# Kernel optimization log

Measured on AMD Instinct MI355X. Metric: run time of the kernel, lower is better.

## Reference

```python
import jax, jax.numpy as jnp
import numpy as np

GROUP = 128  # per-group quantization along the input dimension


def _quantize_int4(w):
    """Asymmetric INT4 per-group quantization. w: [out, in] -> (q, scale, zero).
    q: int32 in [0,15], shape [out, in//GROUP, GROUP]; scale/zero: [out, in//GROUP]."""
    o, i = w.shape
    wg = w.reshape(o, i // GROUP, GROUP)
    mn = wg.min(axis=-1)
    mx = wg.max(axis=-1)
    scale = (mx - mn) / 15.0
    scale = jnp.where(scale == 0, jnp.float32(1.0), scale)
    zero = jnp.clip(jnp.round(-mn / scale), 0.0, 15.0)
    q = jnp.clip(jnp.round(wg / scale[..., None]) + zero[..., None], 0.0, 15.0).astype(jnp.int32)
    return q, scale.astype(jnp.float32), zero.astype(jnp.float32)


def _dequant(q, s, z):
    """(q - zero) * scale, regrouped back to [out, in]."""
    w = (q.astype(jnp.float32) - z[..., None]) * s[..., None]
    return w.reshape(q.shape[0], -1)


def setup_inputs() -> dict:
    key = jax.random.key(0)
    ks = jax.random.split(key, 5)
    B, D_IN, D_H, D_OUT = 512, 2048, 8192, 2048
    x = jax.random.normal(ks[0], (B, D_IN), dtype=jnp.float32)
    w1 = jax.random.normal(ks[1], (D_H, D_IN), dtype=jnp.float32) * 0.02
    b1 = jax.random.normal(ks[2], (D_H,), dtype=jnp.float32) * 0.01
    w2 = jax.random.normal(ks[3], (D_OUT, D_H), dtype=jnp.float32) * 0.02
    b2 = jax.random.normal(ks[4], (D_OUT,), dtype=jnp.float32) * 0.01
    q1, s1, z1 = _quantize_int4(w1)
    q2, s2, z2 = _quantize_int4(w2)
    return {"x": x, "q1": q1, "s1": s1, "z1": z1, "b1": b1,
            "q2": q2, "s2": s2, "z2": z2, "b2": b2}


def reference(x, q1, s1, z1, b1, q2, s2, z2, b2):
    # Layer 1: INT4 dequant + Linear + ReLU (fused in the native kernel)
    w1 = _dequant(q1, s1, z1)              # [D_H, D_IN]
    h = jax.nn.relu(x @ w1.T + b1)         # [B, D_H]
    # Layer 2: INT4 dequant + Linear (no activation)
    w2 = _dequant(q2, s2, z2)              # [D_OUT, D_H]
    return h @ w2.T + b2                   # [B, D_OUT]
```

## Files before the change

### kernel.cpp

```cpp
#include <hip/hip_runtime.h>
#include <stdint.h>

typedef unsigned short u16;
typedef __attribute__((ext_vector_type(8))) short bf16x8;
typedef __attribute__((ext_vector_type(8))) unsigned short u16x8;
typedef __attribute__((ext_vector_type(4))) float f32x4;
typedef __attribute__((ext_vector_type(4))) int i32x4;

__device__ __forceinline__ u16 f2bf(float f) {
  uint32_t u = __builtin_bit_cast(uint32_t, f);
  u += 0x7fffu + ((u >> 16) & 1u);
  return (u16)(u >> 16);
}

#define GLD16(g, l)                                                         \
  __builtin_amdgcn_global_load_lds(                                         \
      (const __attribute__((address_space(1))) void*)(g),                   \
      (__attribute__((address_space(3))) void*)(l), 16, 0, 0)


__global__ __launch_bounds__(256) void cvt_f32_bf16(const float* __restrict__ src,
                                                    u16* __restrict__ dst, int n8) {
  int t = blockIdx.x * 256 + threadIdx.x;
  if (t >= n8) return;
  f32x4 a = ((const f32x4*)src)[2 * t];
  f32x4 b = ((const f32x4*)src)[2 * t + 1];
  u16x8 o;
  o[0] = f2bf(a[0]); o[1] = f2bf(a[1]); o[2] = f2bf(a[2]); o[3] = f2bf(a[3]);
  o[4] = f2bf(b[0]); o[5] = f2bf(b[1]); o[6] = f2bf(b[2]); o[7] = f2bf(b[3]);
  ((u16x8*)dst)[t] = o;
}

__global__ __launch_bounds__(256) void dequant_w(const int* __restrict__ q,
                                                 const float* __restrict__ s,
                                                 const float* __restrict__ z,
                                                 u16* __restrict__ w, int n8) {
  int t = blockIdx.x * 256 + threadIdx.x;
  if (t >= n8) return;
  int g = t >> 4;
  float sc = s[g];
  float zp = z[g];
  i32x4 a = ((const i32x4*)q)[2 * t];
  i32x4 b = ((const i32x4*)q)[2 * t + 1];
  u16x8 o;
  o[0] = f2bf(((float)a[0] - zp) * sc);
  o[1] = f2bf(((float)a[1] - zp) * sc);
  o[2] = f2bf(((float)a[2] - zp) * sc);
  o[3] = f2bf(((float)a[3] - zp) * sc);
  o[4] = f2bf(((float)b[0] - zp) * sc);
  o[5] = f2bf(((float)b[1] - zp) * sc);
  o[6] = f2bf(((float)b[2] - zp) * sc);
  o[7] = f2bf(((float)b[3] - zp) * sc);
  ((u16x8*)w)[t] = o;
}

__global__ __launch_bounds__(256) void bias_init(float* __restrict__ out,
                                                 const float* __restrict__ b,
                                                 int N, int n4) {
  int t = blockIdx.x * 256 + threadIdx.x;
  if (t >= n4) return;
  int idx = t * 4;
  int n = idx & (N - 1);
  *(f32x4*)(out + idx) = *(const f32x4*)(b + n);
}

template <bool RELU, bool OUT_BF16, bool ATOMIC>
__global__ __launch_bounds__(256) void gemm_bt(const u16* __restrict__ A,
                                               const u16* __restrict__ Bm,
                                               const float* __restrict__ bias,
                                               void* __restrict__ Cout,
                                               int M, int N, int K, int kChunk) {
  __shared__ u16 As[3][128 * 32];
  __shared__ u16 Bs[3][128 * 32];
  const int tid = threadIdx.x;
  const int wave = tid >> 6;
  const int lane = tid & 63;
  const int m0 = blockIdx.y << 7;
  const int n0 = blockIdx.x << 7;
  const int kStart = blockIdx.z * kChunk;
  const int srow = lane >> 2;
  const int scol = (((lane & 3) ^ ((lane >> 3) & 3)) << 3);
  const int wm = (wave >> 1) << 6;
  const int wn = (wave & 1) << 6;
  const int quad = lane >> 4;
  const int l15 = lane & 15;
  const int cs = ((quad ^ ((l15 >> 1) & 3)) << 3);

  const u16* Ab = A + (size_t)(m0 + 32 * wave + srow) * K + kStart + scol;
  const u16* Bb = Bm + (size_t)(n0 + 32 * wave + srow) * K + kStart + scol;
  const int ldsW = (32 * wave) * 32;
  const size_t rowskip = (size_t)16 * K;
  const int nT = kChunk >> 5;

  f32x4 acc[4][4];
#pragma unroll
  for (int i = 0; i < 4; i++)
#pragma unroll
    for (int j = 0; j < 4; j++) acc[i][j] = (f32x4){0.f, 0.f, 0.f, 0.f};

#define STAGE(bi_, t_)                                    \
  do {                                                    \
    const int ko_ = (t_) << 5;                            \
    GLD16(Ab + ko_, &As[bi_][ldsW]);                      \
    GLD16(Ab + ko_ + rowskip, &As[bi_][ldsW + 512]);      \
    GLD16(Bb + ko_, &Bs[bi_][ldsW]);                      \
    GLD16(Bb + ko_ + rowskip, &Bs[bi_][ldsW + 512]);      \
  } while (0)

  bf16x8 af[4], bf[4];
#define LOADFRAGS(bi_)                                                        \
  do {                                                                        \
    _Pragma("unroll") for (int i = 0; i < 4; i++)                             \
        af[i] = *(const bf16x8*)&As[bi_][(wm + i * 16 + l15) * 32 + cs];      \
    _Pragma("unroll") for (int j = 0; j < 4; j++)                             \
        bf[j] = *(const bf16x8*)&Bs[bi_][(wn + j * 16 + l15) * 32 + cs];      \
  } while (0)

#define DOMFMA()                                                              \
  do {                                                                        \
    _Pragma("unroll") for (int i = 0; i < 4; i++)                             \
        _Pragma("unroll") for (int j = 0; j < 4; j++)                         \
            acc[i][j] = __builtin_amdgcn_mfma_f32_16x16x32_bf16(              \
                af[i], bf[j], acc[i][j], 0, 0, 0);                            \
  } while (0)

  STAGE(0, 0);
  STAGE(1, 1);
  STAGE(2, 2);

  int bi = 0;
  for (int t = 0; t < nT - 2; ++t) {
    asm volatile("s_waitcnt vmcnt(8)" ::: "memory");
    __builtin_amdgcn_s_barrier();
    LOADFRAGS(bi);
    asm volatile("s_waitcnt lgkmcnt(0)" ::: "memory");
    __builtin_amdgcn_s_barrier();
    if (t + 3 < nT) STAGE(bi, t + 3);
    DOMFMA();
    bi = (bi == 2) ? 0 : bi + 1;
  }
  asm volatile("s_waitcnt vmcnt(4)" ::: "memory");
  __builtin_amdgcn_s_barrier();
  LOADFRAGS(bi);
  DOMFMA();
  bi = (bi == 2) ? 0 : bi + 1;
  asm volatile("s_waitcnt vmcnt(0)" ::: "memory");
  __builtin_amdgcn_s_barrier();
  LOADFRAGS(bi);
  DOMFMA();

#undef STAGE
#undef LOADFRAGS
#undef DOMFMA

#pragma unroll
  for (int i = 0; i < 4; i++) {
#pragma unroll
    for (int j = 0; j < 4; j++) {
      const int col = n0 + wn + j * 16 + l15;
      float bv = 0.f;
      if (!ATOMIC) bv = bias[col];
#pragma unroll
      for (int r = 0; r < 4; r++) {
        const int row = m0 + wm + i * 16 + quad * 4 + r;
        float v = acc[i][j][r];
        if (ATOMIC) {
          atomicAdd((float*)Cout + (size_t)row * N + col, v);
        } else {
          v += bv;
          if (RELU) v = v > 0.f ? v : 0.f;
          if (OUT_BF16)
            ((u16*)Cout)[(size_t)row * N + col] = f2bf(v);
          else
            ((float*)Cout)[(size_t)row * N + col] = v;
        }
      }
    }
  }
}


extern "C" void kernel_launch(void* const* d_in, const int* in_sizes, int n_in,
                              void* d_out, int out_size, void* d_ws, size_t ws_size,
                              hipStream_t stream) {
  const float* x  = (const float*)d_in[0];
  const int*   q1 = (const int*)d_in[1];
  const float* s1 = (const float*)d_in[2];
  const float* z1 = (const float*)d_in[3];
  const float* b1 = (const float*)d_in[4];
  const int*   q2 = (const int*)d_in[5];
  const float* s2 = (const float*)d_in[6];
  const float* z2 = (const float*)d_in[7];
  const float* b2 = (const float*)d_in[8];
  float* out = (float*)d_out;

  const int B = 512, D_IN = 2048, D_H = 8192, D_OUT = 2048;

  char* ws = (char*)d_ws;
  u16* xb  = (u16*)(ws);
  u16* w1b = (u16*)(ws + (size_t)2 * 1024 * 1024);
  u16* hb  = (u16*)(ws + (size_t)34 * 1024 * 1024);
  u16* w2b = (u16*)(ws + (size_t)42 * 1024 * 1024);

  cvt_f32_bf16<<<(B * D_IN / 8 + 255) / 256, 256, 0, stream>>>(x, xb, B * D_IN / 8);
  dequant_w<<<(D_H * D_IN / 8 + 255) / 256, 256, 0, stream>>>(q1, s1, z1, w1b, D_H * D_IN / 8);
  dequant_w<<<(D_OUT * D_H / 8 + 255) / 256, 256, 0, stream>>>(q2, s2, z2, w2b, D_OUT * D_H / 8);
  dim3 g1(D_H / 128, B / 128, 1);
  gemm_bt<true, true, false><<<g1, 256, 0, stream>>>(xb, w1b, b1, hb, B, D_H, D_IN, D_IN);
  bias_init<<<(B * D_OUT / 4 + 255) / 256, 256, 0, stream>>>(out, b2, D_OUT, B * D_OUT / 4);
  dim3 g2(D_OUT / 128, B / 128, 8);
  gemm_bt<false, false, true><<<g2, 256, 0, stream>>>(hb, w2b, nullptr, out, B, D_OUT, D_H, D_H / 8);
}
```

Baseline: 252.9 us.

## Merge dequant launches, narrow GEMM1 N-tile, double-buffer LDS, raise split-K

The two weight dequant launches become one launch with a z-dimension selecting the weight set. The GEMM becomes templated on N-tile width: GEMM1 uses 128x64 tiles to double the block count, and GEMM2's split-K rises from 8 to 16. The LDS pipeline drops from triple to double buffering, with sched_barriers added around the waits. These changes aim for more parallelism and occupancy, but they bring more atomic traffic in GEMM2 and less prefetch depth.

```diff
diff --git a/kernel.cpp b/kernel.cpp
--- a/kernel.cpp
+++ b/kernel.cpp
@@ -31,12 +31,20 @@
   ((u16x8*)dst)[t] = o;
 }
 
-__global__ __launch_bounds__(256) void dequant_w(const int* __restrict__ q,
-                                                 const float* __restrict__ s,
-                                                 const float* __restrict__ z,
-                                                 u16* __restrict__ w, int n8) {
+__global__ __launch_bounds__(256) void dequant_w2x(const int* __restrict__ qa,
+                                                   const float* __restrict__ sa,
+                                                   const float* __restrict__ za,
+                                                   u16* __restrict__ wa,
+                                                   const int* __restrict__ qb,
+                                                   const float* __restrict__ sb,
+                                                   const float* __restrict__ zb,
+                                                   u16* __restrict__ wb, int n8) {
   int t = blockIdx.x * 256 + threadIdx.x;
   if (t >= n8) return;
+  const int* q = blockIdx.z ? qb : qa;
+  const float* s = blockIdx.z ? sb : sa;
+  const float* z = blockIdx.z ? zb : za;
+  u16* w = blockIdx.z ? wb : wa;
   int g = t >> 4;
   float sc = s[g];
   float zp = z[g];
@@ -64,89 +72,92 @@
   *(f32x4*)(out + idx) = *(const f32x4*)(b + n);
 }
 
-template <bool RELU, bool OUT_BF16, bool ATOMIC>
+template <int NJ, bool RELU, bool OUT_BF16, bool ATOMIC>
 __global__ __launch_bounds__(256) void gemm_bt(const u16* __restrict__ A,
                                                const u16* __restrict__ Bm,
                                                const float* __restrict__ bias,
                                                void* __restrict__ Cout,
-                                               int M, int N, int K, int kChunk) {
-  __shared__ u16 As[3][128 * 32];
-  __shared__ u16 Bs[3][128 * 32];
+                                               int N, int K, int kChunk) {
+  __shared__ u16 As[2][128 * 32];
+  __shared__ u16 Bs[2][32 * NJ * 32];
   const int tid = threadIdx.x;
   const int wave = tid >> 6;
   const int lane = tid & 63;
   const int m0 = blockIdx.y << 7;
-  const int n0 = blockIdx.x << 7;
+  const int n0 = blockIdx.x * (32 * NJ);
   const int kStart = blockIdx.z * kChunk;
   const int srow = lane >> 2;
   const int scol = (((lane & 3) ^ ((lane >> 3) & 3)) << 3);
   const int wm = (wave >> 1) << 6;
-  const int wn = (wave & 1) << 6;
+  const int wn = (wave & 1) * (16 * NJ);
   const int quad = lane >> 4;
   const int l15 = lane & 15;
   const int cs = ((quad ^ ((l15 >> 1) & 3)) << 3);
 
   const u16* Ab = A + (size_t)(m0 + 32 * wave + srow) * K + kStart + scol;
-  const u16* Bb = Bm + (size_t)(n0 + 32 * wave + srow) * K + kStart + scol;
-  const int ldsW = (32 * wave) * 32;
+  const u16* Bb = Bm + (size_t)(n0 + (8 * NJ) * wave + srow) * K + kStart + scol;
+  const int ldsA = (32 * wave) * 32;
+  const int ldsB = ((8 * NJ) * wave) * 32;
   const size_t rowskip = (size_t)16 * K;
   const int nT = kChunk >> 5;
-
-  f32x4 acc[4][4];
+  constexpr int VM = 2 + NJ / 2;
+
+  f32x4 acc[4][NJ];
 #pragma unroll
   for (int i = 0; i < 4; i++)
 #pragma unroll
-    for (int j = 0; j < 4; j++) acc[i][j] = (f32x4){0.f, 0.f, 0.f, 0.f};
-
-#define STAGE(bi_, t_)                                    \
-  do {                                                    \
-    const int ko_ = (t_) << 5;                            \
-    GLD16(Ab + ko_, &As[bi_][ldsW]);                      \
-    GLD16(Ab + ko_ + rowskip, &As[bi_][ldsW + 512]);      \
-    GLD16(Bb + ko_, &Bs[bi_][ldsW]);                      \
-    GLD16(Bb + ko_ + rowskip, &Bs[bi_][ldsW + 512]);      \
+    for (int j = 0; j < NJ; j++) acc[i][j] = (f32x4){0.f, 0.f, 0.f, 0.f};
+
+#define STAGE(bi_, t_)                                        \
+  do {                                                        \
+    const int ko_ = (t_) << 5;                                \
+    GLD16(Ab + ko_, &As[bi_][ldsA]);                          \
+    GLD16(Ab + ko_ + rowskip, &As[bi_][ldsA + 512]);          \
+    GLD16(Bb + ko_, &Bs[bi_][ldsB]);                          \
+    if (NJ == 4) GLD16(Bb + ko_ + rowskip, &Bs[bi_][ldsB + 512]); \
   } while (0)
 
-  bf16x8 af[4], bf[4];
+  bf16x8 af[4], bf[NJ];
 #define LOADFRAGS(bi_)                                                        \
   do {                                                                        \
     _Pragma("unroll") for (int i = 0; i < 4; i++)                             \
         af[i] = *(const bf16x8*)&As[bi_][(wm + i * 16 + l15) * 32 + cs];      \
-    _Pragma("unroll") for (int j = 0; j < 4; j++)                             \
+    _Pragma("unroll") for (int j = 0; j < NJ; j++)                            \
         bf[j] = *(const bf16x8*)&Bs[bi_][(wn + j * 16 + l15) * 32 + cs];      \
   } while (0)
 
 #define DOMFMA()                                                              \
   do {                                                                        \
     _Pragma("unroll") for (int i = 0; i < 4; i++)                             \
-        _Pragma("unroll") for (int j = 0; j < 4; j++)                         \
+        _Pragma("unroll") for (int j = 0; j < NJ; j++)                        \
             acc[i][j] = __builtin_amdgcn_mfma_f32_16x16x32_bf16(              \
                 af[i], bf[j], acc[i][j], 0, 0, 0);                            \
   } while (0)
 
   STAGE(0, 0);
   STAGE(1, 1);
-  STAGE(2, 2);
-
-  int bi = 0;
+
   for (int t = 0; t < nT - 2; ++t) {
-    asm volatile("s_waitcnt vmcnt(8)" ::: "memory");
+    asm volatile("s_waitcnt vmcnt(%0)" ::"i"(VM) : "memory");
     __builtin_amdgcn_s_barrier();
-    LOADFRAGS(bi);
+    LOADFRAGS(t & 1);
     asm volatile("s_waitcnt lgkmcnt(0)" ::: "memory");
+    __builtin_amdgcn_sched_barrier(0);
     __builtin_amdgcn_s_barrier();
-    if (t + 3 < nT) STAGE(bi, t + 3);
+    STAGE(t & 1, t + 2);
     DOMFMA();
-    bi = (bi == 2) ? 0 : bi + 1;
-  }
-  asm volatile("s_waitcnt vmcnt(4)" ::: "memory");
+  }
+  asm volatile("s_waitcnt vmcnt(%0)" ::"i"(VM) : "memory");
   __builtin_amdgcn_s_barrier();
-  LOADFRAGS(bi);
+  LOADFRAGS((nT - 2) & 1);
+  asm volatile("s_waitcnt lgkmcnt(0)" ::: "memory");
+  __builtin_amdgcn_sched_barrier(0);
   DOMFMA();
-  bi = (bi == 2) ? 0 : bi + 1;
   asm volatile("s_waitcnt vmcnt(0)" ::: "memory");
   __builtin_amdgcn_s_barrier();
-  LOADFRAGS(bi);
+  LOADFRAGS((nT - 1) & 1);
+  asm volatile("s_waitcnt lgkmcnt(0)" ::: "memory");
+  __builtin_amdgcn_sched_barrier(0);
   DOMFMA();
 
 #undef STAGE
@@ -156,7 +167,7 @@
 #pragma unroll
   for (int i = 0; i < 4; i++) {
 #pragma unroll
-    for (int j = 0; j < 4; j++) {
+    for (int j = 0; j < NJ; j++) {
       const int col = n0 + wn + j * 16 + l15;
       float bv = 0.f;
       if (!ATOMIC) bv = bias[col];
@@ -203,11 +214,20 @@
   u16* w2b = (u16*)(ws + (size_t)42 * 1024 * 1024);
 
   cvt_f32_bf16<<<(B * D_IN / 8 + 255) / 256, 256, 0, stream>>>(x, xb, B * D_IN / 8);
-  dequant_w<<<(D_H * D_IN / 8 + 255) / 256, 256, 0, stream>>>(q1, s1, z1, w1b, D_H * D_IN / 8);
-  dequant_w<<<(D_OUT * D_H / 8 + 255) / 256, 256, 0, stream>>>(q2, s2, z2, w2b, D_OUT * D_H / 8);
-  dim3 g1(D_H / 128, B / 128, 1);
-  gemm_bt<true, true, false><<<g1, 256, 0, stream>>>(xb, w1b, b1, hb, B, D_H, D_IN, D_IN);
+  {
+    const int n8 = D_H * D_IN / 8;
+    dim3 gd((n8 + 255) / 256, 1, 2);
+    dequant_w2x<<<gd, 256, 0, stream>>>(q1, s1, z1, w1b, q2, s2, z2, w2b, n8);
+  }
+  {
+    dim3 g1(D_H / 64, B / 128, 1);
+    gemm_bt<2, true, true, false><<<g1, 256, 0, stream>>>(xb, w1b, b1, hb,
+                                                          D_H, D_IN, D_IN);
+  }
   bias_init<<<(B * D_OUT / 4 + 255) / 256, 256, 0, stream>>>(out, b2, D_OUT, B * D_OUT / 4);
-  dim3 g2(D_OUT / 128, B / 128, 8);
-  gemm_bt<false, false, true><<<g2, 256, 0, stream>>>(hb, w2b, nullptr, out, B, D_OUT, D_H, D_H / 8);
-}
+  {
+    dim3 g2(D_OUT / 128, B / 128, 16);
+    gemm_bt<4, false, false, true><<<g2, 256, 0, stream>>>(hb, w2b, nullptr, out,
+                                                           D_OUT, D_H, D_H / 16);
+  }
+}
```

New measurement: 269.5 us. 1.07x slower.
